# Performance work log

Hardware: AMD Instinct MI355X
Metric: run time of the kernel (lower is better)

The kernel has to match this reference:

```python
import jax, jax.numpy as jnp
import numpy as np

B, S, IN, OUT = 4, 2048, 4096, 12288


def setup_inputs() -> dict:
    key = jax.random.key(0)
    k1, k2, k3, k4 = jax.random.split(key, 4)
    x = jax.random.normal(k1, (B, S, IN), dtype=jnp.float32).astype(jnp.float16)
    # int8 quantized weight in [-127, 127]
    w_q = jax.random.randint(k2, (OUT, IN), -127, 128, dtype=jnp.int32).astype(jnp.int8)
    # per-output-channel dequant scale (fp32, positive, small)
    w_scale = (jax.random.uniform(k3, (OUT, 1), dtype=jnp.float32) + 0.5) * 0.01
    bias = (jax.random.normal(k4, (OUT,), dtype=jnp.float32) * 0.02).astype(jnp.float16)
    return {"x": x, "w_q": w_q, "w_scale": w_scale, "bias": bias}


def reference(x, w_q, w_scale, bias):
    # dynamic per-token activation quantization: scale = absmax / 127
    x32 = x.astype(jnp.float32)
    x_scale = jnp.maximum(jnp.max(jnp.abs(x32), axis=-1, keepdims=True), 1e-6) / 127.0  # [B,S,1]
    x_q = jnp.clip(jnp.round(x32 / x_scale), -128, 127).astype(jnp.int8)  # [B,S,IN]
    acc = jnp.einsum("bsi,oi->bso", x_q, w_q, preferred_element_type=jnp.int32)  # [B,S,OUT]
    # fused dequant (per-token scale * per-channel scale) + bias
    out = acc.astype(jnp.float32) * x_scale * w_scale[:, 0]
    out = out + bias.astype(jnp.float32)
    return out.astype(x.dtype)
```

## Files before the change

### kernel.cpp

```cpp
#include <hip/hip_runtime.h>
#include <hip/hip_fp16.h>
#include <stdint.h>

#define M_TOK 8192
#define K_IN  4096
#define N_OUT 12288

typedef int v4i_t __attribute__((ext_vector_type(4)));

__device__ __forceinline__ void load_lds16(const void* g, void* l) {
    __builtin_amdgcn_global_load_lds(
        (const __attribute__((address_space(1))) unsigned int*)g,
        (__attribute__((address_space(3))) unsigned int*)l, 16, 0, 0);
}

#define PACK_BLOCKS 2048
#define PACK_ITERS  24

__global__ __launch_bounds__(256) void prep_kernel(
    const int* __restrict__ wsrc, uint32_t* __restrict__ wdst,
    const float* __restrict__ x, int8_t* __restrict__ xq, float* __restrict__ xs) {
    const int tid = threadIdx.x;
    const int bid = blockIdx.x;
    if (bid < PACK_BLOCKS) {
        size_t i = (size_t)bid * 256 + tid;
#pragma unroll
        for (int it = 0; it < PACK_ITERS; ++it, i += (size_t)PACK_BLOCKS * 256) {
            const int4 v = ((const int4*)wsrc)[i];
            wdst[i] = (uint32_t)(uint8_t)(int8_t)v.x
                    | ((uint32_t)(uint8_t)(int8_t)v.y << 8)
                    | ((uint32_t)(uint8_t)(int8_t)v.z << 16)
                    | ((uint32_t)(uint8_t)(int8_t)v.w << 24);
        }
        return;
    }
    const int token = bid - PACK_BLOCKS;
    const float4* src = (const float4*)(x + (size_t)token * K_IN);
    float v[16];
#pragma unroll
    for (int c = 0; c < 4; ++c) {
        float4 p = src[c * 256 + tid];
        v[c * 4 + 0] = p.x; v[c * 4 + 1] = p.y;
        v[c * 4 + 2] = p.z; v[c * 4 + 3] = p.w;
    }
    float amax = 0.f;
#pragma unroll
    for (int i = 0; i < 16; ++i) amax = fmaxf(amax, fabsf(v[i]));
#pragma unroll
    for (int off = 32; off >= 1; off >>= 1)
        amax = fmaxf(amax, __shfl_xor(amax, off));
    __shared__ float wmax[4];
    const int wave = tid >> 6, lane = tid & 63;
    if (lane == 0) wmax[wave] = amax;
    __syncthreads();
    amax = fmaxf(fmaxf(wmax[0], wmax[1]), fmaxf(wmax[2], wmax[3]));
    const float scale = fmaxf(amax, 1e-6f) / 127.0f;
    if (tid == 0) xs[token] = scale;

    uint32_t* dst = (uint32_t*)(xq + (size_t)token * K_IN);
#pragma unroll
    for (int c = 0; c < 4; ++c) {
        uint32_t w = 0;
#pragma unroll
        for (int e = 0; e < 4; ++e) {
            float r = rintf(v[c * 4 + e] / scale);
            r = fminf(fmaxf(r, -128.f), 127.f);
            w |= (uint32_t)(uint8_t)(int8_t)(int)r << (8 * e);
        }
        dst[c * 256 + tid] = w;
    }
}

__global__ __launch_bounds__(512, 2) void gemm_kernel(
    const int8_t* __restrict__ xq, const float* __restrict__ xs,
    const int8_t* __restrict__ wq, const float* __restrict__ wscale,
    const float* __restrict__ bias, float* __restrict__ out) {
    extern __shared__ char smem[];

    const int tid  = threadIdx.x;
    const int wid  = tid >> 6, lane = tid & 63;
    const int wr   = wid >> 2, wc = wid & 3;

    const int bid = blockIdx.x;
    const int xcd = bid & 7;
    const int s   = bid >> 3;
    const int g   = s >> 5;
    const int r_  = s & 31;
    const int by  = xcd * 4 + (r_ & 3);
    const int bx  = g * 8 + (r_ >> 2);
    const int m0  = by * 256, n0 = bx * 256;

    const int8_t* Ag = xq + (size_t)m0 * K_IN;
    const int8_t* Bg = wq + (size_t)n0 * K_IN;

    const int rl = (lane >> 2) & 15;
    const int rg = (rl & 0xA) | ((rl & 1) << 2) | ((rl >> 2) & 1);
    const size_t rowByte = (size_t)(wid * 16 + rg) * K_IN;
    const int gsw16 = ((lane & 3) ^ ((lane >> 3) & 3)) << 4;

    const int fr = lane & 15, fq = lane >> 4;
    const int sfr = (fr & 0xA) | ((fr & 1) << 2) | ((fr >> 2) & 1);
    const int frOff = sfr * 64 + (((fq ^ (sfr >> 1)) & 3) << 4);

    auto stage_half = [&](int h) {
        const int th = h >> 2, r = h & 3;
        const int isB = r & 1, kk = r >> 1;
        const int8_t* G = isB ? Bg : Ag;
        char* lb = smem + (isB << 16) + ((((th & 1) << 1) | kk) << 14) + (wid << 10);
        const int8_t* g0 = G + rowByte + th * 128 + (kk << 6) + gsw16;
        load_lds16(g0, lb);
        load_lds16(g0 + (size_t)128 * K_IN, lb + 8192);
    };

    v4i_t acc[8][4] = {};

#pragma unroll
    for (int h = 0; h < 6; ++h) stage_half(h);
    asm volatile("s_waitcnt vmcnt(8)" ::: "memory");
    __builtin_amdgcn_s_barrier();
    __builtin_amdgcn_sched_barrier(0);

    for (int T = 0; T < 32; ++T) {
        const int b   = T & 1;
        const int A0o = b << 15, A1o = A0o + 16384;
        const int B0o = 65536 + A0o, B1o = 65536 + A1o;
        const int h0  = 4 * T + 6;
        const int ab  = (wr << 13) + frOff;
        const int bb  = (wc << 12) + frOff;
        v4i_t af[4], bf[4];

#pragma unroll
        for (int j = 0; j < 4; ++j) bf[j] = *(const v4i_t*)(smem + B0o + bb + (j << 10));
#pragma unroll
        for (int i = 0; i < 4; ++i) af[i] = *(const v4i_t*)(smem + A0o + ab + (i << 10));
        if (h0 < 128) stage_half(h0);
        __builtin_amdgcn_s_barrier();
        asm volatile("s_waitcnt lgkmcnt(0)" ::: "memory");
        __builtin_amdgcn_sched_barrier(0);
        __builtin_amdgcn_s_setprio(1);
#pragma unroll
        for (int i = 0; i < 4; ++i)
#pragma unroll
            for (int j = 0; j < 4; ++j)
                acc[i][j] = __builtin_amdgcn_mfma_i32_16x16x64_i8(af[i], bf[j], acc[i][j], 0, 0, 0);
        __builtin_amdgcn_s_setprio(0);
        __builtin_amdgcn_s_barrier();
        __builtin_amdgcn_sched_barrier(0);

#pragma unroll
        for (int i = 0; i < 4; ++i) af[i] = *(const v4i_t*)(smem + A0o + ab + ((i + 4) << 10));
        if (h0 + 1 < 128) stage_half(h0 + 1);
        __builtin_amdgcn_s_barrier();
        asm volatile("s_waitcnt lgkmcnt(0)" ::: "memory");
        __builtin_amdgcn_sched_barrier(0);
        __builtin_amdgcn_s_setprio(1);
#pragma unroll
        for (int i = 0; i < 4; ++i)
#pragma unroll
            for (int j = 0; j < 4; ++j)
                acc[i + 4][j] = __builtin_amdgcn_mfma_i32_16x16x64_i8(af[i], bf[j], acc[i + 4][j], 0, 0, 0);
        __builtin_amdgcn_s_setprio(0);
        if (T < 31) asm volatile("s_waitcnt vmcnt(8)" ::: "memory");
        else        asm volatile("s_waitcnt vmcnt(0)" ::: "memory");
        __builtin_amdgcn_s_barrier();
        __builtin_amdgcn_sched_barrier(0);

#pragma unroll
        for (int j = 0; j < 4; ++j) bf[j] = *(const v4i_t*)(smem + B1o + bb + (j << 10));
#pragma unroll
        for (int i = 0; i < 4; ++i) af[i] = *(const v4i_t*)(smem + A1o + ab + (i << 10));
        if (h0 + 2 < 128) stage_half(h0 + 2);
        __builtin_amdgcn_s_barrier();
        asm volatile("s_waitcnt lgkmcnt(0)" ::: "memory");
        __builtin_amdgcn_sched_barrier(0);
        __builtin_amdgcn_s_setprio(1);
#pragma unroll
        for (int i = 0; i < 4; ++i)
#pragma unroll
            for (int j = 0; j < 4; ++j)
                acc[i][j] = __builtin_amdgcn_mfma_i32_16x16x64_i8(af[i], bf[j], acc[i][j], 0, 0, 0);
        __builtin_amdgcn_s_setprio(0);
        __builtin_amdgcn_s_barrier();
        __builtin_amdgcn_sched_barrier(0);

#pragma unroll
        for (int i = 0; i < 4; ++i) af[i] = *(const v4i_t*)(smem + A1o + ab + ((i + 4) << 10));
        if (h0 + 3 < 128) stage_half(h0 + 3);
        __builtin_amdgcn_s_barrier();
        asm volatile("s_waitcnt lgkmcnt(0)" ::: "memory");
        __builtin_amdgcn_sched_barrier(0);
        __builtin_amdgcn_s_setprio(1);
#pragma unroll
        for (int i = 0; i < 4; ++i)
#pragma unroll
            for (int j = 0; j < 4; ++j)
                acc[i + 4][j] = __builtin_amdgcn_mfma_i32_16x16x64_i8(af[i], bf[j], acc[i + 4][j], 0, 0, 0);
        __builtin_amdgcn_s_setprio(0);
        if (T < 30)       asm volatile("s_waitcnt vmcnt(8)" ::: "memory");
        else if (T == 30) asm volatile("s_waitcnt vmcnt(4)" ::: "memory");
        __builtin_amdgcn_s_barrier();
        __builtin_amdgcn_sched_barrier(0);
    }

    const int col = lane & 15, rq = lane >> 4;
#pragma unroll
    for (int i = 0; i < 8; ++i) {
        const int mb = m0 + wr * 128 + i * 16 + rq * 4;
        float xsv[4];
#pragma unroll
        for (int r = 0; r < 4; ++r) xsv[r] = xs[mb + r];
#pragma unroll
        for (int j = 0; j < 4; ++j) {
            const int n = n0 + wc * 64 + j * 16 + col;
            const float ws = wscale[n];
            const float bv = bias[n];
#pragma unroll
            for (int r = 0; r < 4; ++r) {
                float o = (float)acc[i][j][r] * xsv[r] * ws + bv;
                o = __half2float(__float2half(o));
                out[(size_t)(mb + r) * N_OUT + n] = o;
            }
        }
    }
}

extern "C" void kernel_launch(void* const* d_in, const int* in_sizes, int n_in,
                              void* d_out, int out_size, void* d_ws, size_t ws_size,
                              hipStream_t stream) {
    const float* x      = (const float*)d_in[0];
    const int*   wq32   = (const int*)d_in[1];
    const float* wscale = (const float*)d_in[2];
    const float* bias   = (const float*)d_in[3];
    float* out = (float*)d_out;

    int8_t* xq  = (int8_t*)d_ws;
    float*  xs  = (float*)((char*)d_ws + (size_t)M_TOK * K_IN);
    int8_t* wq8 = (int8_t*)((char*)d_ws + (size_t)M_TOK * K_IN + 65536);

    static bool attrDone = false;
    if (!attrDone) {
        (void)hipFuncSetAttribute((const void*)gemm_kernel,
                                  hipFuncAttributeMaxDynamicSharedMemorySize, 131072);
        attrDone = true;
    }

    prep_kernel<<<PACK_BLOCKS + M_TOK, 256, 0, stream>>>(wq32, (uint32_t*)wq8, x, xq, xs);

    gemm_kernel<<<dim3(1536), dim3(512), 131072, stream>>>(xq, xs, wq8, wscale, bias, out);
}
```

Measured before the change: 963.1 us.

## Restructure GEMM main loop to one barrier per phase with shallower prefetch

Replaces the four-phase K loop, which used two barriers per phase, with a macro-generated phase that has a single barrier between issuing LDS reads plus the next global-to-LDS stage and the MFMA block. The prologue now stages five half-tiles instead of six, and the vmcnt waits move to phases 0 and 2. The last iteration is peeled so its drain wait is vmcnt(0). The goal is to remove the extra per-phase barrier and tighten the load/compute overlap. The cost is a shallower prefetch lead and a risk of LDS write-after-read hazards, since buffers may be overwritten with fewer synchronisation points.

```diff
diff --git a/kernel.cpp b/kernel.cpp
--- a/kernel.cpp
+++ b/kernel.cpp
@@ -115,92 +115,63 @@
     v4i_t acc[8][4] = {};
 
 #pragma unroll
-    for (int h = 0; h < 6; ++h) stage_half(h);
-    asm volatile("s_waitcnt vmcnt(8)" ::: "memory");
+    for (int h = 0; h < 5; ++h) stage_half(h);
+    asm volatile("s_waitcnt vmcnt(6)" ::: "memory");
+    __builtin_amdgcn_sched_barrier(0);
     __builtin_amdgcn_s_barrier();
     __builtin_amdgcn_sched_barrier(0);
 
-    for (int T = 0; T < 32; ++T) {
-        const int b   = T & 1;
-        const int A0o = b << 15, A1o = A0o + 16384;
-        const int B0o = 65536 + A0o, B1o = 65536 + A1o;
-        const int h0  = 4 * T + 6;
-        const int ab  = (wr << 13) + frOff;
-        const int bb  = (wc << 12) + frOff;
-        v4i_t af[4], bf[4];
-
-#pragma unroll
-        for (int j = 0; j < 4; ++j) bf[j] = *(const v4i_t*)(smem + B0o + bb + (j << 10));
-#pragma unroll
-        for (int i = 0; i < 4; ++i) af[i] = *(const v4i_t*)(smem + A0o + ab + (i << 10));
-        if (h0 < 128) stage_half(h0);
-        __builtin_amdgcn_s_barrier();
-        asm volatile("s_waitcnt lgkmcnt(0)" ::: "memory");
-        __builtin_amdgcn_sched_barrier(0);
-        __builtin_amdgcn_s_setprio(1);
-#pragma unroll
-        for (int i = 0; i < 4; ++i)
-#pragma unroll
-            for (int j = 0; j < 4; ++j)
-                acc[i][j] = __builtin_amdgcn_mfma_i32_16x16x64_i8(af[i], bf[j], acc[i][j], 0, 0, 0);
-        __builtin_amdgcn_s_setprio(0);
-        __builtin_amdgcn_s_barrier();
-        __builtin_amdgcn_sched_barrier(0);
-
-#pragma unroll
-        for (int i = 0; i < 4; ++i) af[i] = *(const v4i_t*)(smem + A0o + ab + ((i + 4) << 10));
-        if (h0 + 1 < 128) stage_half(h0 + 1);
-        __builtin_amdgcn_s_barrier();
-        asm volatile("s_waitcnt lgkmcnt(0)" ::: "memory");
-        __builtin_amdgcn_sched_barrier(0);
-        __builtin_amdgcn_s_setprio(1);
-#pragma unroll
-        for (int i = 0; i < 4; ++i)
-#pragma unroll
-            for (int j = 0; j < 4; ++j)
-                acc[i + 4][j] = __builtin_amdgcn_mfma_i32_16x16x64_i8(af[i], bf[j], acc[i + 4][j], 0, 0, 0);
-        __builtin_amdgcn_s_setprio(0);
-        if (T < 31) asm volatile("s_waitcnt vmcnt(8)" ::: "memory");
-        else        asm volatile("s_waitcnt vmcnt(0)" ::: "memory");
-        __builtin_amdgcn_s_barrier();
-        __builtin_amdgcn_sched_barrier(0);
-
-#pragma unroll
-        for (int j = 0; j < 4; ++j) bf[j] = *(const v4i_t*)(smem + B1o + bb + (j << 10));
-#pragma unroll
-        for (int i = 0; i < 4; ++i) af[i] = *(const v4i_t*)(smem + A1o + ab + (i << 10));
-        if (h0 + 2 < 128) stage_half(h0 + 2);
-        __builtin_amdgcn_s_barrier();
-        asm volatile("s_waitcnt lgkmcnt(0)" ::: "memory");
-        __builtin_amdgcn_sched_barrier(0);
-        __builtin_amdgcn_s_setprio(1);
-#pragma unroll
-        for (int i = 0; i < 4; ++i)
-#pragma unroll
-            for (int j = 0; j < 4; ++j)
-                acc[i][j] = __builtin_amdgcn_mfma_i32_16x16x64_i8(af[i], bf[j], acc[i][j], 0, 0, 0);
-        __builtin_amdgcn_s_setprio(0);
-        __builtin_amdgcn_s_barrier();
-        __builtin_amdgcn_sched_barrier(0);
-
-#pragma unroll
-        for (int i = 0; i < 4; ++i) af[i] = *(const v4i_t*)(smem + A1o + ab + ((i + 4) << 10));
-        if (h0 + 3 < 128) stage_half(h0 + 3);
-        __builtin_amdgcn_s_barrier();
-        asm volatile("s_waitcnt lgkmcnt(0)" ::: "memory");
-        __builtin_amdgcn_sched_barrier(0);
-        __builtin_amdgcn_s_setprio(1);
-#pragma unroll
-        for (int i = 0; i < 4; ++i)
-#pragma unroll
-            for (int j = 0; j < 4; ++j)
-                acc[i + 4][j] = __builtin_amdgcn_mfma_i32_16x16x64_i8(af[i], bf[j], acc[i + 4][j], 0, 0, 0);
-        __builtin_amdgcn_s_setprio(0);
-        if (T < 30)       asm volatile("s_waitcnt vmcnt(8)" ::: "memory");
-        else if (T == 30) asm volatile("s_waitcnt vmcnt(4)" ::: "memory");
-        __builtin_amdgcn_s_barrier();
-        __builtin_amdgcn_sched_barrier(0);
-    }
+    v4i_t af[4], bf[4];
+
+#define PHASE(T_, PH_, LAST_)                                                          \
+    {                                                                                  \
+        const int kk_   = (PH_) >> 1;                                                  \
+        const int slab_ = ((((T_) & 1) << 1) | kk_) << 14;                             \
+        const int ioff_ = ((PH_) & 1) * 4;                                             \
+        if (((PH_) & 1) == 0) {                                                        \
+            _Pragma("unroll")                                                          \
+            for (int j = 0; j < 4; ++j)                                                \
+                bf[j] = *(const v4i_t*)(smem + 65536 + slab_ + (wc << 12) + frOff + (j << 10)); \
+        }                                                                              \
+        _Pragma("unroll")                                                              \
+        for (int i = 0; i < 4; ++i)                                                    \
+            af[i] = *(const v4i_t*)(smem + slab_ + (wr << 13) + frOff + ((ioff_ + i) << 10)); \
+        const int hs_ = 4 * (T_) + 5 + (PH_);                                          \
+        if (hs_ < 128) stage_half(hs_);                                                \
+        __builtin_amdgcn_sched_barrier(0);                                             \
+        __builtin_amdgcn_s_barrier();                                                  \
+        asm volatile("s_waitcnt lgkmcnt(0)" ::: "memory");                             \
+        __builtin_amdgcn_sched_barrier(0);                                             \
+        __builtin_amdgcn_s_setprio(1);                                                 \
+        _Pragma("unroll")                                                              \
+        for (int i = 0; i < 4; ++i)                                                    \
+            _Pragma("unroll")                                                          \
+            for (int j = 0; j < 4; ++j)                                                \
+                acc[ioff_ + i][j] =                                                    \
+                    __builtin_amdgcn_mfma_i32_16x16x64_i8(af[i], bf[j], acc[ioff_ + i][j], 0, 0, 0); \
+        __builtin_amdgcn_s_setprio(0);                                                 \
+        if ((PH_) == 0) {                                                              \
+            if (LAST_) asm volatile("s_waitcnt vmcnt(0)" ::: "memory");                \
+            else       asm volatile("s_waitcnt vmcnt(4)" ::: "memory");                \
+            __builtin_amdgcn_sched_barrier(0);                                         \
+        }                                                                              \
+        if ((PH_) == 2 && !(LAST_)) {                                                  \
+            asm volatile("s_waitcnt vmcnt(4)" ::: "memory");                           \
+            __builtin_amdgcn_sched_barrier(0);                                         \
+        }                                                                              \
+    }
+
+    for (int T = 0; T < 31; ++T) {
+        PHASE(T, 0, false)
+        PHASE(T, 1, false)
+        PHASE(T, 2, false)
+        PHASE(T, 3, false)
+    }
+    PHASE(31, 0, true)
+    PHASE(31, 1, true)
+    PHASE(31, 2, true)
+    PHASE(31, 3, true)
+#undef PHASE
 
     const int col = lane & 15, rq = lane >> 4;
 #pragma unroll
```

New measurement: 943.2 us. 1.02x faster.
